# Optimization experiments

Measured on AMD Instinct MI355X. Metric: run time of the kernel, lower is better.

The kernel has to match this reference:

```python
import jax, jax.numpy as jnp
import numpy as np

B, H, W, C, HEADS = 8, 64, 64, 128, 4
H_SP, W_SP = 64, 8            # idx=0: H_sp = H, W_sp = split_size
HD = C // HEADS               # 32
N = H_SP * W_SP               # 512 tokens per window
SCALE = HD ** -0.5


def setup_inputs() -> dict:
    key = jax.random.key(0)
    k1, k2, k3 = jax.random.split(key, 3)
    return {
        "qkv": jax.random.normal(k1, (3, B, H * W, C), dtype=jnp.float32),
        "conv_w": jax.random.normal(k2, (C, 1, 3, 3), dtype=jnp.float32) * 0.1,
        "conv_b": jax.random.normal(k3, (C,), dtype=jnp.float32) * 0.1,
    }


def _to_windows(x):
    # x: [B, L, C] -> window tokens [Bw, N, C] with Bw = B * (H//H_SP) * (W//W_SP)
    x = x.reshape(B, H // H_SP, H_SP, W // W_SP, W_SP, C)
    x = x.transpose(0, 1, 3, 2, 4, 5).reshape(-1, N, C)
    return x


def _heads(x):
    # [Bw, N, C] -> [Bw, heads, N, hd]
    return x.reshape(-1, N, HEADS, HD).transpose(0, 2, 1, 3)


def reference(qkv, conv_w, conv_b):
    q, k, v = qkv[0], qkv[1], qkv[2]

    qw = _heads(_to_windows(q)) * SCALE   # [Bw, h, N, hd]
    kw = _heads(_to_windows(k))

    vwin = _to_windows(v)                 # [Bw, N, C]
    # LePE: depthwise 3x3 conv on each window (NHWC, feature_group_count=C)
    vimg = vwin.reshape(-1, H_SP, W_SP, C)
    w_hwio = conv_w.transpose(2, 3, 1, 0)  # [3,3,1,C]
    lepe = jax.lax.conv_general_dilated(
        vimg, w_hwio, window_strides=(1, 1), padding='SAME',
        dimension_numbers=('NHWC', 'HWIO', 'NHWC'), feature_group_count=C,
    ) + conv_b
    lepe = _heads(lepe.reshape(-1, N, C))  # [Bw, h, N, hd]
    vw = _heads(vwin)

    attn = jax.nn.softmax(jnp.einsum('whqd,whkd->whqk', qw, kw), axis=-1)
    out = jnp.einsum('whqk,whkd->whqd', attn, vw) + lepe  # [Bw, h, N, hd]

    # merge heads and windows back to [B, L, C]
    out = out.transpose(0, 2, 1, 3).reshape(-1, N, C)
    out = out.reshape(B, H // H_SP, W // W_SP, H_SP, W_SP, C)
    out = out.transpose(0, 1, 3, 2, 4, 5).reshape(B, H * W, C)
    return out
```

## Files before the change

### kernel.cpp

```cpp
#include <hip/hip_runtime.h>


namespace {
constexpr int Bn   = 8;
constexpr int Ww   = 64;
constexpr int Cc   = 128;
constexpr int HD   = 32;
constexpr int WSP  = 8;
constexpr int NTOK = 512;
constexpr int LL   = 64 * 64;
constexpr float SCALE_L2E = 0.17677669529663687f * 1.4426950408889634f;
constexpr int KPAD = 40;
constexpr int VPAD = 536;
}

typedef __bf16 bf16x8 __attribute__((ext_vector_type(8)));
typedef float  f32x16 __attribute__((ext_vector_type(16)));
typedef unsigned int uint32x4 __attribute__((ext_vector_type(4)));

__device__ inline unsigned cvtpk(float x, float y) {
    unsigned r;
    asm("v_cvt_pk_bf16_f32 %0, %1, %2" : "=v"(r) : "v"(x), "v"(y));
    return r;
}

__global__ __launch_bounds__(512, 4) void attn_kernel(const float* __restrict__ qkv,
                                                      const float* __restrict__ cw,
                                                      const float* __restrict__ cb,
                                                      float* __restrict__ out) {
    const int blk = blockIdx.x;
    const int w   = blk >> 3;
    const int h   = (blk >> 1) & 3;
    const int qh  = blk & 1;
    const int b   = w >> 3;
    const int wb  = w & 7;
    const int tid = threadIdx.x;
    const int wv  = tid >> 6;
    const int lane = tid & 63;
    const int l31 = lane & 31;
    const int h5  = lane >> 5;

    const float* qp = qkv;
    const float* kp = qkv + (size_t)Bn * LL * Cc;
    const float* vp = qkv + (size_t)2 * Bn * LL * Cc;

    __shared__ short K_lds[NTOK][KPAD];
    __shared__ short VT_lds[HD][VPAD];

    const int qtok = qh * 256 + wv * 32 + l31;
    const int qlqi = (qtok >> 3) * Ww + wb * WSP + (qtok & 7);
    bf16x8 qf[2];
    {
        const float* p = qp + ((size_t)b * LL + qlqi) * Cc + h * HD + h5 * 8;
#pragma unroll
        for (int dc = 0; dc < 2; ++dc) {
            float4 a = *reinterpret_cast<const float4*>(p + dc * 16);
            float4 c = *reinterpret_cast<const float4*>(p + dc * 16 + 4);
            uint32x4 u;
            u.x = cvtpk(a.x * SCALE_L2E, a.y * SCALE_L2E);
            u.y = cvtpk(a.z * SCALE_L2E, a.w * SCALE_L2E);
            u.z = cvtpk(c.x * SCALE_L2E, c.y * SCALE_L2E);
            u.w = cvtpk(c.z * SCALE_L2E, c.w * SCALE_L2E);
            qf[dc] = __builtin_bit_cast(bf16x8, u);
        }
    }

    for (int i = tid; i < (NTOK / 2) * 8; i += 512) {
        const int tp = i >> 3, j = i & 7;
        const int t0 = tp * 2, t1 = t0 + 1;
        const int lqi0 = (t0 >> 3) * Ww + wb * WSP + (t0 & 7);
        const size_t b0 = ((size_t)b * LL + lqi0) * Cc + h * HD + j * 4;
        const float4 k0 = *reinterpret_cast<const float4*>(kp + b0);
        const float4 k1 = *reinterpret_cast<const float4*>(kp + b0 + Cc);
        uint2 pk0, pk1;
        pk0.x = cvtpk(k0.x, k0.y);  pk0.y = cvtpk(k0.z, k0.w);
        pk1.x = cvtpk(k1.x, k1.y);  pk1.y = cvtpk(k1.z, k1.w);
        *reinterpret_cast<uint2*>(&K_lds[t0][j * 4]) = pk0;
        *reinterpret_cast<uint2*>(&K_lds[t1][j * 4]) = pk1;
        const float4 v0 = *reinterpret_cast<const float4*>(vp + b0);
        const float4 v1 = *reinterpret_cast<const float4*>(vp + b0 + Cc);
        *reinterpret_cast<unsigned*>(&VT_lds[j * 4 + 0][t0]) = cvtpk(v0.x, v1.x);
        *reinterpret_cast<unsigned*>(&VT_lds[j * 4 + 1][t0]) = cvtpk(v0.y, v1.y);
        *reinterpret_cast<unsigned*>(&VT_lds[j * 4 + 2][t0]) = cvtpk(v0.z, v1.z);
        *reinterpret_cast<unsigned*>(&VT_lds[j * 4 + 3][t0]) = cvtpk(v0.w, v1.w);
    }
    __syncthreads();

    f32x16 acc  = (f32x16)(0.f);
    f32x16 lacc = (f32x16)(0.f);
    const f32x16 z16 = (f32x16)(0.f);

    uint32x4 onesu;
    onesu.x = 0x3F803F80u; onesu.y = 0x3F803F80u;
    onesu.z = 0x3F803F80u; onesu.w = 0x3F803F80u;
    const bf16x8 onesf = __builtin_bit_cast(bf16x8, onesu);

    auto load_kf = [&](int kt, bf16x8* kf) {
        const int krow = kt * 32 + l31;
#pragma unroll
        for (int dc = 0; dc < 2; ++dc)
            kf[dc] = __builtin_bit_cast(bf16x8,
                *reinterpret_cast<const uint32x4*>(&K_lds[krow][dc * 16 + h5 * 8]));
    };
    auto load_vu = [&](int kt, uint32x4* vu) {
#pragma unroll
        for (int kw = 0; kw < 2; ++kw) {
            const int kcol = kt * 32 + kw * 16 + h5 * 8;
            vu[kw] = *reinterpret_cast<const uint32x4*>(&VT_lds[l31][kcol]);
        }
    };

    bf16x8 kf[2];
    uint32x4 vu[2];
    load_kf(0, kf);
    load_vu(0, vu);

    for (int kt = 0; kt < 16; ++kt) {
        f32x16 s = z16;
        s = __builtin_amdgcn_mfma_f32_32x32x16_bf16(kf[0], qf[0], s, 0, 0, 0);
        s = __builtin_amdgcn_mfma_f32_32x32x16_bf16(kf[1], qf[1], s, 0, 0, 0);

        bf16x8 kfn[2];
        uint32x4 vun[2];
        load_kf((kt + 1) & 15, kfn);
        load_vu((kt + 1) & 15, vun);

        float pe[16];
#pragma unroll
        for (int i = 0; i < 16; ++i) pe[i] = __builtin_amdgcn_exp2f(s[i]);
        unsigned dw[8];
#pragma unroll
        for (int i = 0; i < 8; ++i) dw[i] = cvtpk(pe[2 * i], pe[2 * i + 1]);

#pragma unroll
        for (int kw = 0; kw < 2; ++kw) {
            unsigned a0 = dw[4 * kw + 0], b0 = dw[4 * kw + 2];
            unsigned a1 = dw[4 * kw + 1], b1 = dw[4 * kw + 3];
            asm("v_permlane32_swap_b32 %0, %1" : "+v"(a0), "+v"(b0));
            asm("v_permlane32_swap_b32 %0, %1" : "+v"(a1), "+v"(b1));
            uint32x4 pu; pu.x = a0; pu.y = a1; pu.z = b0; pu.w = b1;
            const bf16x8 pf = __builtin_bit_cast(bf16x8, pu);
            acc  = __builtin_amdgcn_mfma_f32_32x32x16_bf16(
                pf, __builtin_bit_cast(bf16x8, vu[kw]), acc, 0, 0, 0);
            lacc = __builtin_amdgcn_mfma_f32_32x32x16_bf16(
                pf, onesf, lacc, 0, 0, 0);
        }
        kf[0] = kfn[0];
        kf[1] = kfn[1];
        vu[0] = vun[0];
        vu[1] = vun[1];
    }

    const int ch = h * HD + l31;
    float wreg[9];
#pragma unroll
    for (int wi = 0; wi < 9; ++wi) wreg[wi] = cw[ch * 9 + wi];
    const float bias = cb[ch];

    const int tok0 = qh * 256 + wv * 32;
    unsigned hw[26];
    {
        const int segbase = tok0 + 4 * h5 - 12;
#pragma unroll
        for (int c2 = 0; c2 < 13; ++c2) {
            int t = segbase + 4 * c2;
            t = t < 0 ? 0 : (t > NTOK - 4 ? NTOK - 4 : t);
            const uint2 u = *reinterpret_cast<const uint2*>(&VT_lds[l31][t]);
            hw[c2 * 2 + 0] = u.x;
            hw[c2 * 2 + 1] = u.y;
        }
    }

#pragma unroll
    for (int r = 0; r < 16; ++r) {
        const int c_r = (r & 3) + 8 * (r >> 2);
        const float iv = __builtin_amdgcn_rcpf(lacc[r]);
        const int tok = tok0 + c_r + 4 * h5;
        float cv = bias;
#pragma unroll
        for (int dy = -1; dy <= 1; ++dy) {
            const bool rowok = (unsigned)(tok + dy * 8) < (unsigned)NTOK;
#pragma unroll
            for (int dx = -1; dx <= 1; ++dx) {
                const int idx = c_r + 12 + dy * 8 + dx;
                const unsigned word = hw[idx >> 1];
                const float tap = __builtin_bit_cast(float,
                    (idx & 1) ? (word & 0xFFFF0000u) : (word << 16));
                bool ok = rowok;
                if (dx == -1) ok = ok && (((r & 3) != 0) || (h5 != 0));
                if (dx == +1) ok = ok && (((r & 3) != 3) || (h5 == 0));
                cv += ok ? wreg[(dy + 1) * 3 + (dx + 1)] * tap : 0.f;
            }
        }
        const int lqi = (tok >> 3) * Ww + wb * WSP + (tok & 7);
        out[((size_t)b * LL + lqi) * Cc + ch] = acc[r] * iv + cv;
    }
}

extern "C" void kernel_launch(void* const* d_in, const int* in_sizes, int n_in,
                              void* d_out, int out_size, void* d_ws, size_t ws_size,
                              hipStream_t stream) {
    const float* qkv = (const float*)d_in[0];
    const float* cw  = (const float*)d_in[1];
    const float* cb  = (const float*)d_in[2];
    float* out = (float*)d_out;

    attn_kernel<<<512, 512, 0, stream>>>(qkv, cw, cb, out);
}
```

Measured before the change: 32.08 us.

## Process two query tiles per wave, halving blocks and K/V staging

Each block now covers all 512 query tokens of a window-head instead of half, so each wave computes two 32-row query tiles against every K/V tile it loads from LDS. This halves the redundant global K/V loads and bf16 conversion into LDS, and it shares the K and V fragment loads between two score/PV chains. The cost is doubled accumulator registers (launch bounds lowered to 2 blocks per CU), fewer blocks (256) for the GPU, and V loads that are no longer prefetched one step ahead.

```diff
diff --git a/kernel.cpp b/kernel.cpp
--- a/kernel.cpp
+++ b/kernel.cpp
@@ -24,14 +24,13 @@
     return r;
 }
 
-__global__ __launch_bounds__(512, 4) void attn_kernel(const float* __restrict__ qkv,
+__global__ __launch_bounds__(512, 2) void attn_kernel(const float* __restrict__ qkv,
                                                       const float* __restrict__ cw,
                                                       const float* __restrict__ cb,
                                                       float* __restrict__ out) {
     const int blk = blockIdx.x;
-    const int w   = blk >> 3;
-    const int h   = (blk >> 1) & 3;
-    const int qh  = blk & 1;
+    const int w   = blk >> 2;
+    const int h   = blk & 3;
     const int b   = w >> 3;
     const int wb  = w & 7;
     const int tid = threadIdx.x;
@@ -47,21 +46,28 @@
     __shared__ short K_lds[NTOK][KPAD];
     __shared__ short VT_lds[HD][VPAD];
 
-    const int qtok = qh * 256 + wv * 32 + l31;
-    const int qlqi = (qtok >> 3) * Ww + wb * WSP + (qtok & 7);
-    bf16x8 qf[2];
+    bf16x8 qf00, qf01, qf10, qf11;
     {
-        const float* p = qp + ((size_t)b * LL + qlqi) * Cc + h * HD + h5 * 8;
-#pragma unroll
-        for (int dc = 0; dc < 2; ++dc) {
-            float4 a = *reinterpret_cast<const float4*>(p + dc * 16);
-            float4 c = *reinterpret_cast<const float4*>(p + dc * 16 + 4);
-            uint32x4 u;
-            u.x = cvtpk(a.x * SCALE_L2E, a.y * SCALE_L2E);
-            u.y = cvtpk(a.z * SCALE_L2E, a.w * SCALE_L2E);
-            u.z = cvtpk(c.x * SCALE_L2E, c.y * SCALE_L2E);
-            u.w = cvtpk(c.z * SCALE_L2E, c.w * SCALE_L2E);
-            qf[dc] = __builtin_bit_cast(bf16x8, u);
+#pragma unroll
+        for (int qt = 0; qt < 2; ++qt) {
+            const int qtok = wv * 64 + qt * 32 + l31;
+            const int qlqi = (qtok >> 3) * Ww + wb * WSP + (qtok & 7);
+            const float* p = qp + ((size_t)b * LL + qlqi) * Cc + h * HD + h5 * 8;
+#pragma unroll
+            for (int dc = 0; dc < 2; ++dc) {
+                float4 a = *reinterpret_cast<const float4*>(p + dc * 16);
+                float4 c = *reinterpret_cast<const float4*>(p + dc * 16 + 4);
+                uint32x4 u;
+                u.x = cvtpk(a.x * SCALE_L2E, a.y * SCALE_L2E);
+                u.y = cvtpk(a.z * SCALE_L2E, a.w * SCALE_L2E);
+                u.z = cvtpk(c.x * SCALE_L2E, c.y * SCALE_L2E);
+                u.w = cvtpk(c.z * SCALE_L2E, c.w * SCALE_L2E);
+                const bf16x8 qv = __builtin_bit_cast(bf16x8, u);
+                if (qt == 0 && dc == 0) qf00 = qv;
+                if (qt == 0 && dc == 1) qf01 = qv;
+                if (qt == 1 && dc == 0) qf10 = qv;
+                if (qt == 1 && dc == 1) qf11 = qv;
+            }
         }
     }
 
@@ -86,8 +92,8 @@
     }
     __syncthreads();
 
-    f32x16 acc  = (f32x16)(0.f);
-    f32x16 lacc = (f32x16)(0.f);
+    f32x16 acc0  = (f32x16)(0.f), acc1  = (f32x16)(0.f);
+    f32x16 lacc0 = (f32x16)(0.f), lacc1 = (f32x16)(0.f);
     const f32x16 z16 = (f32x16)(0.f);
 
     uint32x4 onesu;
@@ -109,29 +115,14 @@
             vu[kw] = *reinterpret_cast<const uint32x4*>(&VT_lds[l31][kcol]);
         }
     };
-
-    bf16x8 kf[2];
-    uint32x4 vu[2];
-    load_kf(0, kf);
-    load_vu(0, vu);
-
-    for (int kt = 0; kt < 16; ++kt) {
-        f32x16 s = z16;
-        s = __builtin_amdgcn_mfma_f32_32x32x16_bf16(kf[0], qf[0], s, 0, 0, 0);
-        s = __builtin_amdgcn_mfma_f32_32x32x16_bf16(kf[1], qf[1], s, 0, 0, 0);
-
-        bf16x8 kfn[2];
-        uint32x4 vun[2];
-        load_kf((kt + 1) & 15, kfn);
-        load_vu((kt + 1) & 15, vun);
-
+    auto softmax_pv = [&](const f32x16& s, const uint32x4* vu,
+                          f32x16& accR, f32x16& laccR) {
         float pe[16];
 #pragma unroll
         for (int i = 0; i < 16; ++i) pe[i] = __builtin_amdgcn_exp2f(s[i]);
         unsigned dw[8];
 #pragma unroll
         for (int i = 0; i < 8; ++i) dw[i] = cvtpk(pe[2 * i], pe[2 * i + 1]);
-
 #pragma unroll
         for (int kw = 0; kw < 2; ++kw) {
             unsigned a0 = dw[4 * kw + 0], b0 = dw[4 * kw + 2];
@@ -140,15 +131,33 @@
             asm("v_permlane32_swap_b32 %0, %1" : "+v"(a1), "+v"(b1));
             uint32x4 pu; pu.x = a0; pu.y = a1; pu.z = b0; pu.w = b1;
             const bf16x8 pf = __builtin_bit_cast(bf16x8, pu);
-            acc  = __builtin_amdgcn_mfma_f32_32x32x16_bf16(
-                pf, __builtin_bit_cast(bf16x8, vu[kw]), acc, 0, 0, 0);
-            lacc = __builtin_amdgcn_mfma_f32_32x32x16_bf16(
-                pf, onesf, lacc, 0, 0, 0);
-        }
+            accR  = __builtin_amdgcn_mfma_f32_32x32x16_bf16(
+                pf, __builtin_bit_cast(bf16x8, vu[kw]), accR, 0, 0, 0);
+            laccR = __builtin_amdgcn_mfma_f32_32x32x16_bf16(
+                pf, onesf, laccR, 0, 0, 0);
+        }
+    };
+
+    bf16x8 kf[2];
+    load_kf(0, kf);
+
+    for (int kt = 0; kt < 16; ++kt) {
+        f32x16 s0 = z16, s1 = z16;
+        s0 = __builtin_amdgcn_mfma_f32_32x32x16_bf16(kf[0], qf00, s0, 0, 0, 0);
+        s0 = __builtin_amdgcn_mfma_f32_32x32x16_bf16(kf[1], qf01, s0, 0, 0, 0);
+        s1 = __builtin_amdgcn_mfma_f32_32x32x16_bf16(kf[0], qf10, s1, 0, 0, 0);
+        s1 = __builtin_amdgcn_mfma_f32_32x32x16_bf16(kf[1], qf11, s1, 0, 0, 0);
+
+        bf16x8 kfn[2];
+        load_kf((kt + 1) & 15, kfn);
+        uint32x4 vu[2];
+        load_vu(kt, vu);
+
+        softmax_pv(s0, vu, acc0, lacc0);
+        softmax_pv(s1, vu, acc1, lacc1);
+
         kf[0] = kfn[0];
         kf[1] = kfn[1];
-        vu[0] = vun[0];
-        vu[1] = vun[1];
     }
 
     const int ch = h * HD + l31;
@@ -157,9 +166,8 @@
     for (int wi = 0; wi < 9; ++wi) wreg[wi] = cw[ch * 9 + wi];
     const float bias = cb[ch];
 
-    const int tok0 = qh * 256 + wv * 32;
-    unsigned hw[26];
-    {
+    auto do_epi = [&](int tok0, const f32x16& accR, const f32x16& laccR) {
+        unsigned hw[26];
         const int segbase = tok0 + 4 * h5 - 12;
 #pragma unroll
         for (int c2 = 0; c2 < 13; ++c2) {
@@ -169,32 +177,34 @@
             hw[c2 * 2 + 0] = u.x;
             hw[c2 * 2 + 1] = u.y;
         }
-    }
-
-#pragma unroll
-    for (int r = 0; r < 16; ++r) {
-        const int c_r = (r & 3) + 8 * (r >> 2);
-        const float iv = __builtin_amdgcn_rcpf(lacc[r]);
-        const int tok = tok0 + c_r + 4 * h5;
-        float cv = bias;
-#pragma unroll
-        for (int dy = -1; dy <= 1; ++dy) {
-            const bool rowok = (unsigned)(tok + dy * 8) < (unsigned)NTOK;
-#pragma unroll
-            for (int dx = -1; dx <= 1; ++dx) {
-                const int idx = c_r + 12 + dy * 8 + dx;
-                const unsigned word = hw[idx >> 1];
-                const float tap = __builtin_bit_cast(float,
-                    (idx & 1) ? (word & 0xFFFF0000u) : (word << 16));
-                bool ok = rowok;
-                if (dx == -1) ok = ok && (((r & 3) != 0) || (h5 != 0));
-                if (dx == +1) ok = ok && (((r & 3) != 3) || (h5 == 0));
-                cv += ok ? wreg[(dy + 1) * 3 + (dx + 1)] * tap : 0.f;
+#pragma unroll
+        for (int r = 0; r < 16; ++r) {
+            const int c_r = (r & 3) + 8 * (r >> 2);
+            const float iv = __builtin_amdgcn_rcpf(laccR[r]);
+            const int tok = tok0 + c_r + 4 * h5;
+            float cv = bias;
+#pragma unroll
+            for (int dy = -1; dy <= 1; ++dy) {
+                const bool rowok = (unsigned)(tok + dy * 8) < (unsigned)NTOK;
+#pragma unroll
+                for (int dx = -1; dx <= 1; ++dx) {
+                    const int idx = c_r + 12 + dy * 8 + dx;
+                    const unsigned word = hw[idx >> 1];
+                    const float tap = __builtin_bit_cast(float,
+                        (idx & 1) ? (word & 0xFFFF0000u) : (word << 16));
+                    bool ok = rowok;
+                    if (dx == -1) ok = ok && (((r & 3) != 0) || (h5 != 0));
+                    if (dx == +1) ok = ok && (((r & 3) != 3) || (h5 == 0));
+                    cv += ok ? wreg[(dy + 1) * 3 + (dx + 1)] * tap : 0.f;
+                }
             }
-        }
-        const int lqi = (tok >> 3) * Ww + wb * WSP + (tok & 7);
-        out[((size_t)b * LL + lqi) * Cc + ch] = acc[r] * iv + cv;
-    }
+            const int lqi = (tok >> 3) * Ww + wb * WSP + (tok & 7);
+            out[((size_t)b * LL + lqi) * Cc + ch] = accR[r] * iv + cv;
+        }
+    };
+
+    do_epi(wv * 64, acc0, lacc0);
+    do_epi(wv * 64 + 32, acc1, lacc1);
 }
 
 extern "C" void kernel_launch(void* const* d_in, const int* in_sizes, int n_in,
@@ -205,5 +215,5 @@
     const float* cb  = (const float*)d_in[2];
     float* out = (float*)d_out;
 
-    attn_kernel<<<512, 512, 0, stream>>>(qkv, cw, cb, out);
-}
+    attn_kernel<<<256, 512, 0, stream>>>(qkv, cw, cb, out);
+}
```

Result: no change. 32.13 us (+0.2%).
